# Kernel optimization log

Measured on AMD Instinct MI355X. Metric: run time of the kernel, lower is better.

Reference implementation:

```python
import jax, jax.numpy as jnp
import numpy as np

ALPHA = 1.0
GAMMA = 2.0            # initial_focal_gamma (epoch 0)
DIST_THRESHOLD = 0.1
WEIGHT_FACTOR = 2.0
DISTANCE_WEIGHT = 1.0


def setup_inputs() -> dict:
    key = jax.random.key(0)
    k1, k2, k3, k4 = jax.random.split(key, 4)
    B, N, C, M = 64, 16384, 6, 128
    inputs = jax.random.normal(k1, (B, N), dtype=jnp.float32)
    targets = (jax.random.uniform(k2, (B, N)) < 0.05).astype(jnp.float32)
    point_coords = jax.random.uniform(k3, (B, N, C), dtype=jnp.float32)
    corner_coords = jax.random.uniform(k4, (B, M, 3), dtype=jnp.float32)
    # mark last 32 corners per sample invalid (sentinel -1), exercising the mask
    invalid = jnp.arange(M) >= (M - 32)
    corner_coords = jnp.where(invalid[None, :, None], -1.0, corner_coords)
    return {"inputs": inputs, "targets": targets,
            "point_coords": point_coords, "corner_coords": corner_coords}


def _bce_with_logits(logits, targets):
    # stable: max(x,0) - x*t + log(1+exp(-|x|))
    return jnp.maximum(logits, 0.0) - logits * targets + jnp.log1p(jnp.exp(-jnp.abs(logits)))


def _focal_elementwise(inputs, targets):
    ce = _bce_with_logits(inputs, targets)
    probs = jax.nn.sigmoid(inputs)
    p_t = probs * targets + (1.0 - probs) * (1.0 - targets)
    return ALPHA * (1.0 - p_t) ** GAMMA * ce  # [B, N]


def reference(inputs, targets, point_coords, corner_coords):
    # focal loss (mean reduction)
    focal_elem = _focal_elementwise(inputs, targets)
    focal_loss = focal_elem.mean()

    # distance-weighted loss: 1-NN distance from each point to valid corners
    pts = point_coords[..., :3]                          # [B, N, 3]
    valid = corner_coords[..., 0] > -1.0                 # [B, M]
    pts_sq = jnp.sum(pts * pts, axis=-1)                 # [B, N]
    cor_sq = jnp.sum(corner_coords * corner_coords, axis=-1)  # [B, M]
    cross = jnp.einsum('bnc,bmc->bnm', pts, corner_coords)    # [B, N, M]
    d2 = pts_sq[:, :, None] + cor_sq[:, None, :] - 2.0 * cross
    d2 = jnp.maximum(d2, 1e-12)
    d2 = jnp.where(valid[:, None, :], d2, jnp.inf)       # mask invalid corners
    min_d = jnp.sqrt(jnp.min(d2, axis=-1))               # [B, N]; inf if no valid corners
    dist_w = jnp.exp(-min_d / DIST_THRESHOLD)            # 0 when min_d = inf
    weights = 1.0 + WEIGHT_FACTOR * dist_w
    distance_loss = (focal_elem * weights).mean()

    total_loss = focal_loss + DISTANCE_WEIGHT * distance_loss
    return total_loss, focal_loss, distance_loss
```

## Files before the change

kernel.cpp:

```cpp
#include <hip/hip_runtime.h>
#include <math.h>

#define BLOCK 256
#define PPT 4
#define MCOR 128
constexpr int Bb = 64;
constexpr int Nn = 16384;
constexpr int CCH = 6;

__global__ __launch_bounds__(BLOCK) void acl_main(
    const float* __restrict__ inputs,
    const float* __restrict__ targets,
    const float* __restrict__ pts,
    const float* __restrict__ corners,
    float2* __restrict__ partials)
{
    __shared__ float4 cs[MCOR];
    __shared__ float2 wsum[BLOCK / 64];

    const int b   = blockIdx.y;
    const int tid = threadIdx.x;

    if (tid < MCOR) {
        const float* c = corners + ((size_t)b * MCOR + tid) * 3;
        float cx = c[0], cy = c[1], cz = c[2];
        float csq = (cx > -1.0f) ? (cx*cx + cy*cy + cz*cz) : __builtin_inff();
        cs[tid] = make_float4(-2.0f*cx, -2.0f*cy, -2.0f*cz, csq);
    }
    __syncthreads();

    const int n0 = blockIdx.x * (BLOCK * PPT) + tid * PPT;
    const size_t base = (size_t)b * Nn + n0;

    const float4 x4 = *(const float4*)(inputs  + base);
    const float4 t4 = *(const float4*)(targets + base);
    const float4* pv = (const float4*)(pts + base * CCH);
    float4 v0 = pv[0], v1 = pv[1], v2 = pv[2], v3 = pv[3], v4 = pv[4], v5 = pv[5];

    float px[PPT] = {v0.x, v1.z, v3.x, v4.z};
    float py[PPT] = {v0.y, v1.w, v3.y, v4.w};
    float pz[PPT] = {v0.z, v2.x, v3.z, v5.x};

    float dmin[PPT] = {__builtin_inff(), __builtin_inff(), __builtin_inff(), __builtin_inff()};

    #pragma unroll 8
    for (int m = 0; m < MCOR; m += 2) {
        float4 c0 = cs[m];
        float4 c1 = cs[m + 1];
        #pragma unroll
        for (int j = 0; j < PPT; ++j) {
            float t0 = fmaf(c0.x, px[j], fmaf(c0.y, py[j], fmaf(c0.z, pz[j], c0.w)));
            float t1 = fmaf(c1.x, px[j], fmaf(c1.y, py[j], fmaf(c1.z, pz[j], c1.w)));
            dmin[j] = fminf(dmin[j], fminf(t0, t1));
        }
    }

    const float xs[PPT] = {x4.x, x4.y, x4.z, x4.w};
    const float ts[PPT] = {t4.x, t4.y, t4.z, t4.w};
    float fs = 0.0f, ds = 0.0f;
    #pragma unroll
    for (int j = 0; j < PPT; ++j) {
        float psq = fmaf(px[j], px[j], fmaf(py[j], py[j], pz[j]*pz[j]));
        float d2  = fmaxf(psq + dmin[j], 1e-12f);
        float md  = sqrtf(d2);
        float w   = fmaf(2.0f, __expf(-10.0f * md), 1.0f);

        float x = xs[j], t = ts[j];
        float ax = fabsf(x);
        float ce = fmaxf(x, 0.0f) - x*t + __logf(1.0f + __expf(-ax));
        float p  = 1.0f / (1.0f + __expf(-x));
        float pt = p*t + (1.0f - p)*(1.0f - t);
        float om = 1.0f - pt;
        float fe = om * om * ce;

        fs += fe;
        ds = fmaf(fe, w, ds);
    }

    #pragma unroll
    for (int off = 32; off > 0; off >>= 1) {
        fs += __shfl_down(fs, off, 64);
        ds += __shfl_down(ds, off, 64);
    }
    const int wave = tid >> 6, lane = tid & 63;
    if (lane == 0) wsum[wave] = make_float2(fs, ds);
    __syncthreads();
    if (tid == 0) {
        float F = 0.0f, D = 0.0f;
        #pragma unroll
        for (int w = 0; w < BLOCK / 64; ++w) { F += wsum[w].x; D += wsum[w].y; }
        partials[(size_t)blockIdx.y * gridDim.x + blockIdx.x] = make_float2(F, D);
    }
}

__global__ __launch_bounds__(256) void acl_final(
    const float2* __restrict__ partials, int n, float* __restrict__ out)
{
    double f = 0.0, d = 0.0;
    for (int i = threadIdx.x; i < n; i += 256) {
        float2 p = partials[i];
        f += (double)p.x;
        d += (double)p.y;
    }
    #pragma unroll
    for (int off = 32; off > 0; off >>= 1) {
        f += __shfl_down(f, off, 64);
        d += __shfl_down(d, off, 64);
    }
    __shared__ double sf[4], sd[4];
    const int wave = threadIdx.x >> 6, lane = threadIdx.x & 63;
    if (lane == 0) { sf[wave] = f; sd[wave] = d; }
    __syncthreads();
    if (threadIdx.x == 0) {
        double F = sf[0] + sf[1] + sf[2] + sf[3];
        double D = sd[0] + sd[1] + sd[2] + sd[3];
        double inv = 1.0 / ((double)Bb * (double)Nn);
        float focal = (float)(F * inv);
        float dist  = (float)(D * inv);
        out[0] = focal + dist;
        out[1] = focal;
        out[2] = dist;
    }
}

extern "C" void kernel_launch(void* const* d_in, const int* in_sizes, int n_in,
                              void* d_out, int out_size, void* d_ws, size_t ws_size,
                              hipStream_t stream) {
    const float* inputs  = (const float*)d_in[0];
    const float* targets = (const float*)d_in[1];
    const float* pts     = (const float*)d_in[2];
    const float* corners = (const float*)d_in[3];
    float* out = (float*)d_out;
    float2* partials = (float2*)d_ws;

    dim3 grid(Nn / (BLOCK * PPT), Bb);
    acl_main<<<grid, BLOCK, 0, stream>>>(inputs, targets, pts, corners, partials);
    acl_final<<<1, 256, 0, stream>>>(partials, grid.x * grid.y, out);
}
```

Measured before the change: 21.24 us.

## Fuse final reduction via last-block atomic counter and pack distance FMAs

Merges the separate final-reduction kernel into the main kernel. Each block bumps an atomic counter after writing its partial, and the last block to arrive sums all partials in double precision. The counter is reset with a memset on each launch. The nearest-corner loop is also rewritten with 2-wide float vectors so the compiler can emit packed FMA and min instructions, and its unroll is lowered from 8 to 4. This removes one kernel launch but adds a memset, an atomic and fences, and the last block serialises the final sum.

```diff
diff --git a/kernel.cpp b/kernel.cpp
--- a/kernel.cpp
+++ b/kernel.cpp
@@ -1,5 +1,7 @@
 #include <hip/hip_runtime.h>
 #include <math.h>
+
+typedef float f32x2 __attribute__((ext_vector_type(2)));
 
 #define BLOCK 256
 #define PPT 4
@@ -7,16 +9,23 @@
 constexpr int Bb = 64;
 constexpr int Nn = 16384;
 constexpr int CCH = 6;
+constexpr int GRIDX = Nn / (BLOCK * PPT);
+constexpr int NBLK  = GRIDX * Bb;
 
-__global__ __launch_bounds__(BLOCK) void acl_main(
+static __device__ __forceinline__ f32x2 splat2(float s) { return f32x2{s, s}; }
+
+__global__ __launch_bounds__(BLOCK) void acl_fused(
     const float* __restrict__ inputs,
     const float* __restrict__ targets,
     const float* __restrict__ pts,
     const float* __restrict__ corners,
-    float2* __restrict__ partials)
+    float2* __restrict__ partials,
+    unsigned int* __restrict__ counter,
+    float* __restrict__ out)
 {
     __shared__ float4 cs[MCOR];
     __shared__ float2 wsum[BLOCK / 64];
+    __shared__ int is_last;
 
     const int b   = blockIdx.y;
     const int tid = threadIdx.x;
@@ -35,33 +44,45 @@
     const float4 x4 = *(const float4*)(inputs  + base);
     const float4 t4 = *(const float4*)(targets + base);
     const float4* pv = (const float4*)(pts + base * CCH);
-    float4 v0 = pv[0], v1 = pv[1], v2 = pv[2], v3 = pv[3], v4 = pv[4], v5 = pv[5];
+    const float4 v0 = pv[0], v1 = pv[1], v2 = pv[2];
+    const float4 v3 = pv[3], v4 = pv[4], v5 = pv[5];
 
-    float px[PPT] = {v0.x, v1.z, v3.x, v4.z};
-    float py[PPT] = {v0.y, v1.w, v3.y, v4.w};
-    float pz[PPT] = {v0.z, v2.x, v3.z, v5.x};
+    f32x2 PX[2], PY[2], PZ[2], dmin[2];
+    PX[0] = f32x2{v0.x, v1.z};  PX[1] = f32x2{v3.x, v4.z};
+    PY[0] = f32x2{v0.y, v1.w};  PY[1] = f32x2{v3.y, v4.w};
+    PZ[0] = f32x2{v0.z, v2.x};  PZ[1] = f32x2{v3.z, v5.x};
+    dmin[0] = splat2(__builtin_inff());
+    dmin[1] = splat2(__builtin_inff());
 
-    float dmin[PPT] = {__builtin_inff(), __builtin_inff(), __builtin_inff(), __builtin_inff()};
-
-    #pragma unroll 8
+    #pragma unroll 4
     for (int m = 0; m < MCOR; m += 2) {
-        float4 c0 = cs[m];
-        float4 c1 = cs[m + 1];
+        const float4 c0 = cs[m];
+        const float4 c1 = cs[m + 1];
         #pragma unroll
-        for (int j = 0; j < PPT; ++j) {
-            float t0 = fmaf(c0.x, px[j], fmaf(c0.y, py[j], fmaf(c0.z, pz[j], c0.w)));
-            float t1 = fmaf(c1.x, px[j], fmaf(c1.y, py[j], fmaf(c1.z, pz[j], c1.w)));
-            dmin[j] = fminf(dmin[j], fminf(t0, t1));
+        for (int q = 0; q < 2; ++q) {
+            f32x2 t0 = __builtin_elementwise_fma(splat2(c0.x), PX[q],
+                       __builtin_elementwise_fma(splat2(c0.y), PY[q],
+                       __builtin_elementwise_fma(splat2(c0.z), PZ[q], splat2(c0.w))));
+            f32x2 t1 = __builtin_elementwise_fma(splat2(c1.x), PX[q],
+                       __builtin_elementwise_fma(splat2(c1.y), PY[q],
+                       __builtin_elementwise_fma(splat2(c1.z), PZ[q], splat2(c1.w))));
+            dmin[q] = __builtin_elementwise_min(dmin[q],
+                      __builtin_elementwise_min(t0, t1));
         }
     }
 
+    const float px[PPT] = {PX[0].x, PX[0].y, PX[1].x, PX[1].y};
+    const float py[PPT] = {PY[0].x, PY[0].y, PY[1].x, PY[1].y};
+    const float pz[PPT] = {PZ[0].x, PZ[0].y, PZ[1].x, PZ[1].y};
+    const float dm[PPT] = {dmin[0].x, dmin[0].y, dmin[1].x, dmin[1].y};
     const float xs[PPT] = {x4.x, x4.y, x4.z, x4.w};
     const float ts[PPT] = {t4.x, t4.y, t4.z, t4.w};
+
     float fs = 0.0f, ds = 0.0f;
     #pragma unroll
     for (int j = 0; j < PPT; ++j) {
         float psq = fmaf(px[j], px[j], fmaf(py[j], py[j], pz[j]*pz[j]));
-        float d2  = fmaxf(psq + dmin[j], 1e-12f);
+        float d2  = fmaxf(psq + dm[j], 1e-12f);
         float md  = sqrtf(d2);
         float w   = fmaf(2.0f, __expf(-10.0f * md), 1.0f);
 
@@ -85,41 +106,45 @@
     const int wave = tid >> 6, lane = tid & 63;
     if (lane == 0) wsum[wave] = make_float2(fs, ds);
     __syncthreads();
+
     if (tid == 0) {
         float F = 0.0f, D = 0.0f;
         #pragma unroll
         for (int w = 0; w < BLOCK / 64; ++w) { F += wsum[w].x; D += wsum[w].y; }
         partials[(size_t)blockIdx.y * gridDim.x + blockIdx.x] = make_float2(F, D);
+        __threadfence();
+        unsigned prev = atomicAdd(counter, 1u);
+        is_last = (prev == (unsigned)NBLK - 1u);
     }
-}
+    __syncthreads();
 
-__global__ __launch_bounds__(256) void acl_final(
-    const float2* __restrict__ partials, int n, float* __restrict__ out)
-{
-    double f = 0.0, d = 0.0;
-    for (int i = threadIdx.x; i < n; i += 256) {
-        float2 p = partials[i];
-        f += (double)p.x;
-        d += (double)p.y;
-    }
-    #pragma unroll
-    for (int off = 32; off > 0; off >>= 1) {
-        f += __shfl_down(f, off, 64);
-        d += __shfl_down(d, off, 64);
-    }
-    __shared__ double sf[4], sd[4];
-    const int wave = threadIdx.x >> 6, lane = threadIdx.x & 63;
-    if (lane == 0) { sf[wave] = f; sd[wave] = d; }
-    __syncthreads();
-    if (threadIdx.x == 0) {
-        double F = sf[0] + sf[1] + sf[2] + sf[3];
-        double D = sd[0] + sd[1] + sd[2] + sd[3];
-        double inv = 1.0 / ((double)Bb * (double)Nn);
-        float focal = (float)(F * inv);
-        float dist  = (float)(D * inv);
-        out[0] = focal + dist;
-        out[1] = focal;
-        out[2] = dist;
+    if (is_last) {
+        __threadfence();
+        double f = 0.0, d = 0.0;
+        for (int i = tid; i < NBLK; i += BLOCK) {
+            float2 p = partials[i];
+            f += (double)p.x;
+            d += (double)p.y;
+        }
+        #pragma unroll
+        for (int off = 32; off > 0; off >>= 1) {
+            f += __shfl_down(f, off, 64);
+            d += __shfl_down(d, off, 64);
+        }
+        __shared__ double sf[BLOCK / 64], sd[BLOCK / 64];
+        if (lane == 0) { sf[wave] = f; sd[wave] = d; }
+        __syncthreads();
+        if (tid == 0) {
+            double F = 0.0, D = 0.0;
+            #pragma unroll
+            for (int w = 0; w < BLOCK / 64; ++w) { F += sf[w]; D += sd[w]; }
+            const double inv = 1.0 / ((double)Bb * (double)Nn);
+            float focal = (float)(F * inv);
+            float dist  = (float)(D * inv);
+            out[0] = focal + dist;
+            out[1] = focal;
+            out[2] = dist;
+        }
     }
 }
 
@@ -131,9 +156,13 @@
     const float* pts     = (const float*)d_in[2];
     const float* corners = (const float*)d_in[3];
     float* out = (float*)d_out;
-    float2* partials = (float2*)d_ws;
 
-    dim3 grid(Nn / (BLOCK * PPT), Bb);
-    acl_main<<<grid, BLOCK, 0, stream>>>(inputs, targets, pts, corners, partials);
-    acl_final<<<1, 256, 0, stream>>>(partials, grid.x * grid.y, out);
+    unsigned int* counter = (unsigned int*)d_ws;
+    float2* partials = (float2*)((char*)d_ws + 16);
+
+    hipMemsetAsync(counter, 0, sizeof(unsigned int), stream);
+
+    dim3 grid(GRIDX, Bb);
+    acl_fused<<<grid, BLOCK, 0, stream>>>(inputs, targets, pts, corners,
+                                          partials, counter, out);
 }
```

Result: slower. 36.77 us (+73.1%).

## Use packed f32x2 FMA/min for corner distance loop with 8 points per thread

Applied to the files above, without the earlier changes.

Doubles points per thread to 8 and rewrites the nearest-corner inner loop with two-wide float vectors, so the compiler can emit packed FMA and min instructions and reuse each LDS corner read across more points. This targets the ALU-bound distance search. In exchange it halves the grid (1024 blocks), raises register pressure, and makes the final reduction loop bound a compile-time constant.

```diff
diff --git a/kernel.cpp b/kernel.cpp
--- a/kernel.cpp
+++ b/kernel.cpp
@@ -1,12 +1,17 @@
 #include <hip/hip_runtime.h>
 #include <math.h>
 
+typedef float f32x2 __attribute__((ext_vector_type(2)));
+
 #define BLOCK 256
-#define PPT 4
+#define PPT 8
 #define MCOR 128
 constexpr int Bb = 64;
 constexpr int Nn = 16384;
-constexpr int CCH = 6;
+constexpr int GRIDX = Nn / (BLOCK * PPT);
+constexpr int NPART = GRIDX * Bb;
+
+static __device__ __forceinline__ f32x2 splat2(float s) { return f32x2{s, s}; }
 
 __global__ __launch_bounds__(BLOCK) void acl_main(
     const float* __restrict__ inputs,
@@ -32,36 +37,55 @@
     const int n0 = blockIdx.x * (BLOCK * PPT) + tid * PPT;
     const size_t base = (size_t)b * Nn + n0;
 
-    const float4 x4 = *(const float4*)(inputs  + base);
-    const float4 t4 = *(const float4*)(targets + base);
-    const float4* pv = (const float4*)(pts + base * CCH);
-    float4 v0 = pv[0], v1 = pv[1], v2 = pv[2], v3 = pv[3], v4 = pv[4], v5 = pv[5];
+    const float4* xv = (const float4*)(inputs  + base);
+    const float4* tv = (const float4*)(targets + base);
+    const float4* pv = (const float4*)(pts + base * 6);
+    const float4 x0 = xv[0], x1 = xv[1];
+    const float4 t0v = tv[0], t1v = tv[1];
+    float4 v[12];
+    #pragma unroll
+    for (int k = 0; k < 12; ++k) v[k] = pv[k];
 
-    float px[PPT] = {v0.x, v1.z, v3.x, v4.z};
-    float py[PPT] = {v0.y, v1.w, v3.y, v4.w};
-    float pz[PPT] = {v0.z, v2.x, v3.z, v5.x};
+    const float pxs[PPT] = {v[0].x, v[1].z, v[3].x, v[4].z, v[6].x, v[7].z, v[9].x, v[10].z};
+    const float pys[PPT] = {v[0].y, v[1].w, v[3].y, v[4].w, v[6].y, v[7].w, v[9].y, v[10].w};
+    const float pzs[PPT] = {v[0].z, v[2].x, v[3].z, v[5].x, v[6].z, v[8].x, v[9].z, v[11].x};
 
-    float dmin[PPT] = {__builtin_inff(), __builtin_inff(), __builtin_inff(), __builtin_inff()};
+    f32x2 PX[4], PY[4], PZ[4], dmin[4];
+    #pragma unroll
+    for (int q = 0; q < 4; ++q) {
+        PX[q] = f32x2{pxs[2*q], pxs[2*q+1]};
+        PY[q] = f32x2{pys[2*q], pys[2*q+1]};
+        PZ[q] = f32x2{pzs[2*q], pzs[2*q+1]};
+        dmin[q] = splat2(__builtin_inff());
+    }
 
-    #pragma unroll 8
+    #pragma unroll 4
     for (int m = 0; m < MCOR; m += 2) {
-        float4 c0 = cs[m];
-        float4 c1 = cs[m + 1];
+        const float4 c0 = cs[m];
+        const float4 c1 = cs[m + 1];
         #pragma unroll
-        for (int j = 0; j < PPT; ++j) {
-            float t0 = fmaf(c0.x, px[j], fmaf(c0.y, py[j], fmaf(c0.z, pz[j], c0.w)));
-            float t1 = fmaf(c1.x, px[j], fmaf(c1.y, py[j], fmaf(c1.z, pz[j], c1.w)));
-            dmin[j] = fminf(dmin[j], fminf(t0, t1));
+        for (int q = 0; q < 4; ++q) {
+            f32x2 u0 = __builtin_elementwise_fma(splat2(c0.x), PX[q],
+                       __builtin_elementwise_fma(splat2(c0.y), PY[q],
+                       __builtin_elementwise_fma(splat2(c0.z), PZ[q], splat2(c0.w))));
+            f32x2 u1 = __builtin_elementwise_fma(splat2(c1.x), PX[q],
+                       __builtin_elementwise_fma(splat2(c1.y), PY[q],
+                       __builtin_elementwise_fma(splat2(c1.z), PZ[q], splat2(c1.w))));
+            dmin[q] = __builtin_elementwise_min(dmin[q],
+                      __builtin_elementwise_min(u0, u1));
         }
     }
 
-    const float xs[PPT] = {x4.x, x4.y, x4.z, x4.w};
-    const float ts[PPT] = {t4.x, t4.y, t4.z, t4.w};
+    const float dm[PPT] = {dmin[0].x, dmin[0].y, dmin[1].x, dmin[1].y,
+                           dmin[2].x, dmin[2].y, dmin[3].x, dmin[3].y};
+    const float xs[PPT] = {x0.x, x0.y, x0.z, x0.w, x1.x, x1.y, x1.z, x1.w};
+    const float ts[PPT] = {t0v.x, t0v.y, t0v.z, t0v.w, t1v.x, t1v.y, t1v.z, t1v.w};
+
     float fs = 0.0f, ds = 0.0f;
     #pragma unroll
     for (int j = 0; j < PPT; ++j) {
-        float psq = fmaf(px[j], px[j], fmaf(py[j], py[j], pz[j]*pz[j]));
-        float d2  = fmaxf(psq + dmin[j], 1e-12f);
+        float psq = fmaf(pxs[j], pxs[j], fmaf(pys[j], pys[j], pzs[j]*pzs[j]));
+        float d2  = fmaxf(psq + dm[j], 1e-12f);
         float md  = sqrtf(d2);
         float w   = fmaf(2.0f, __expf(-10.0f * md), 1.0f);
 
@@ -94,10 +118,10 @@
 }
 
 __global__ __launch_bounds__(256) void acl_final(
-    const float2* __restrict__ partials, int n, float* __restrict__ out)
+    const float2* __restrict__ partials, float* __restrict__ out)
 {
     double f = 0.0, d = 0.0;
-    for (int i = threadIdx.x; i < n; i += 256) {
+    for (int i = threadIdx.x; i < NPART; i += 256) {
         float2 p = partials[i];
         f += (double)p.x;
         d += (double)p.y;
@@ -133,7 +157,7 @@
     float* out = (float*)d_out;
     float2* partials = (float2*)d_ws;
 
-    dim3 grid(Nn / (BLOCK * PPT), Bb);
+    dim3 grid(GRIDX, Bb);
     acl_main<<<grid, BLOCK, 0, stream>>>(inputs, targets, pts, corners, partials);
-    acl_final<<<1, 256, 0, stream>>>(partials, grid.x * grid.y, out);
+    acl_final<<<1, 256, 0, stream>>>(partials, out);
 }
```

Result: no change. 21.60 us (+1.7%).
